# Optimization experiments

Measured on AMD Instinct MI355X. Metric: run time of the kernel, lower is better.

Reference implementation:

```python
import jax, jax.numpy as jnp
import numpy as np


def setup_inputs() -> dict:
    key = jax.random.key(0)
    k1, k2 = jax.random.split(key)
    B, C, Q, D = 32, 4096, 512, 512
    similarity_matrix = jax.random.normal(k1, (B, C, Q), dtype=jnp.float32)
    encoded_question = jax.random.normal(k2, (B, Q, D), dtype=jnp.float32)
    return {"similarity_matrix": similarity_matrix, "encoded_question": encoded_question}


def reference(similarity_matrix, encoded_question):
    # softmax over query axis, then attention-weighted sum of question encodings.
    # Equivalent to the original expand_dims/multiply/sum, but fused as a matmul.
    attn = jax.nn.softmax(similarity_matrix, axis=-1)          # [B, C, Q]
    out = jnp.einsum('bcq,bqd->bcd', attn, encoded_question)   # [B, C, D]
    return out
```

## Files before the change

### kernel.cpp

```cpp
#include <hip/hip_runtime.h>
#include <hip/hip_bf16.h>


constexpr int Bn = 32;
constexpr int Cn = 4096;
constexpr int Qn = 512;
constexpr int Dn = 512;
constexpr int BM = 64;

typedef __attribute__((ext_vector_type(8))) short short8;
typedef __attribute__((ext_vector_type(4))) float floatx4;

__device__ __forceinline__ ushort f2bf(float f) {
  union { float f; unsigned u; } v; v.f = f;
  unsigned r = v.u + 0x7FFFu + ((v.u >> 16) & 1u);
  return (ushort)(r >> 16);
}

__global__ __launch_bounds__(256) void transpose_conv(const float* __restrict__ E,
                                                      ushort* __restrict__ Et) {
  __shared__ float tile[32][33];
  int b = blockIdx.z, q0 = blockIdx.y * 32, d0 = blockIdx.x * 32;
  int x = threadIdx.x & 31, y = threadIdx.x >> 5;
  const float* src = E + ((size_t)b * Qn + q0) * Dn + d0;
#pragma unroll
  for (int k = 0; k < 4; ++k)
    tile[y + 8 * k][x] = src[(size_t)(y + 8 * k) * Dn + x];
  __syncthreads();
  ushort* dst = Et + ((size_t)b * Dn + d0) * Qn + q0;
#pragma unroll
  for (int k = 0; k < 4; ++k)
    dst[(size_t)(y + 8 * k) * Qn + x] = f2bf(tile[x][y + 8 * k]);
}

__global__ __launch_bounds__(512, 4) void c2q_fused(const float* __restrict__ sim,
                                                    const ushort* __restrict__ Et,
                                                    float* __restrict__ out) {
  __shared__ char Plds[BM * Qn * 2];
  __shared__ float rsInv[BM];

  const int tid  = threadIdx.x;
  const int lane = tid & 63;
  const int wid  = tid >> 6;
  const int l16  = lane & 15;
  const int lhi  = lane >> 4;
  const int b    = blockIdx.y;
  const int c0   = blockIdx.x * BM;

  const int srow = tid >> 3;
  const int skp  = tid & 7;
  const float* sload = sim + ((size_t)b * Cn + c0 + srow) * Qn + skp * 8;

  float4 v[16];
#pragma unroll
  for (int c = 0; c < 8; ++c) {
    v[2 * c]     = *(const float4*)(sload + c * 64);
    v[2 * c + 1] = *(const float4*)(sload + c * 64 + 4);
  }
  float rsum = 0.0f;
#pragma unroll
  for (int c = 0; c < 8; ++c) {
    float e0 = __expf(v[2 * c].x),     e1 = __expf(v[2 * c].y);
    float e2 = __expf(v[2 * c].z),     e3 = __expf(v[2 * c].w);
    float e4 = __expf(v[2 * c + 1].x), e5 = __expf(v[2 * c + 1].y);
    float e6 = __expf(v[2 * c + 1].z), e7 = __expf(v[2 * c + 1].w);
    rsum += ((e0 + e1) + (e2 + e3)) + ((e4 + e5) + (e6 + e7));
    uint4 pk;
    pk.x = (uint)f2bf(e0) | ((uint)f2bf(e1) << 16);
    pk.y = (uint)f2bf(e2) | ((uint)f2bf(e3) << 16);
    pk.z = (uint)f2bf(e4) | ((uint)f2bf(e5) << 16);
    pk.w = (uint)f2bf(e6) | ((uint)f2bf(e7) << 16);
    int off = (srow << 10) + (c << 7) + (skp << 4);
    off ^= (srow & 7) << 4;
    *(uint4*)(Plds + off) = pk;
  }
  rsum += __shfl_xor(rsum, 1);
  rsum += __shfl_xor(rsum, 2);
  rsum += __shfl_xor(rsum, 4);
  if (skp == 0) rsInv[srow] = 1.0f / rsum;
  __syncthreads();

  floatx4 acc[4][4] = {};
  const ushort* EtB = Et + ((size_t)b * Dn + wid * 64 + l16) * Qn + lhi * 8;

  short8 bb[4], nb[4];
#pragma unroll
  for (int nr = 0; nr < 4; ++nr)
    bb[nr] = *(const short8*)(EtB + (size_t)nr * 16 * Qn);

#pragma unroll
  for (int ks = 0; ks < 16; ++ks) {
    if (ks < 15) {
#pragma unroll
      for (int nr = 0; nr < 4; ++nr)
        nb[nr] = *(const short8*)(EtB + (size_t)nr * 16 * Qn + (ks + 1) * 32);
    }
    short8 a[4];
#pragma unroll
    for (int mr = 0; mr < 4; ++mr) {
      int row = mr * 16 + l16;
      int off = (row << 10) + (ks << 6) + (lhi << 4);
      off ^= (row & 7) << 4;
      a[mr] = *(const short8*)(Plds + off);
    }
    __builtin_amdgcn_s_setprio(1);
#pragma unroll
    for (int mr = 0; mr < 4; ++mr)
#pragma unroll
      for (int nr = 0; nr < 4; ++nr)
        acc[mr][nr] = __builtin_amdgcn_mfma_f32_16x16x32_bf16(a[mr], bb[nr],
                                                              acc[mr][nr], 0, 0, 0);
    __builtin_amdgcn_s_setprio(0);
#pragma unroll
    for (int nr = 0; nr < 4; ++nr) bb[nr] = nb[nr];
  }

  float* outp = out + ((size_t)b * Cn + c0) * Dn;
#pragma unroll
  for (int mr = 0; mr < 4; ++mr) {
    float rs[4];
#pragma unroll
    for (int rr = 0; rr < 4; ++rr) rs[rr] = rsInv[mr * 16 + lhi * 4 + rr];
#pragma unroll
    for (int nr = 0; nr < 4; ++nr) {
      int col = wid * 64 + nr * 16 + l16;
#pragma unroll
      for (int rr = 0; rr < 4; ++rr) {
        int row = mr * 16 + lhi * 4 + rr;
        outp[(size_t)row * Dn + col] = acc[mr][nr][rr] * rs[rr];
      }
    }
  }
}

extern "C" void kernel_launch(void* const* d_in, const int* in_sizes, int n_in,
                              void* d_out, int out_size, void* d_ws, size_t ws_size,
                              hipStream_t stream) {
  const float* sim = (const float*)d_in[0];
  const float* enc = (const float*)d_in[1];
  float* outp = (float*)d_out;
  ushort* Et = (ushort*)d_ws;

  transpose_conv<<<dim3(Dn / 32, Qn / 32, Bn), 256, 0, stream>>>(enc, Et);
  c2q_fused<<<dim3(Cn / BM, Bn), 512, 0, stream>>>(sim, Et, outp);
}
```

Baseline: 205.1 us.

## Make c2q blocks persistent over row subtiles with double-buffered softmax staging

```diff
diff --git a/kernel.cpp b/kernel.cpp
--- a/kernel.cpp
+++ b/kernel.cpp
@@ -6,7 +6,9 @@
 constexpr int Cn = 4096;
 constexpr int Qn = 512;
 constexpr int Dn = 512;
-constexpr int BM = 64;
+constexpr int BM = 32;
+constexpr int NSUB = 8;
+constexpr int ROWS = BM * NSUB;
 
 typedef __attribute__((ext_vector_type(8))) short short8;
 typedef __attribute__((ext_vector_type(4))) float floatx4;
@@ -36,100 +38,123 @@
 __global__ __launch_bounds__(512, 4) void c2q_fused(const float* __restrict__ sim,
                                                     const ushort* __restrict__ Et,
                                                     float* __restrict__ out) {
-  __shared__ char Plds[BM * Qn * 2];
-  __shared__ float rsInv[BM];
+  __shared__ char Pbuf[2][BM * Qn * 2];
+  __shared__ float rsInv[2][BM];
 
   const int tid  = threadIdx.x;
   const int lane = tid & 63;
   const int wid  = tid >> 6;
   const int l16  = lane & 15;
   const int lhi  = lane >> 4;
-  const int b    = blockIdx.y;
-  const int c0   = blockIdx.x * BM;
 
-  const int srow = tid >> 3;
-  const int skp  = tid & 7;
-  const float* sload = sim + ((size_t)b * Cn + c0 + srow) * Qn + skp * 8;
+  const int b  = blockIdx.x & 31;
+  const int c0 = (blockIdx.x >> 5) * ROWS;
 
-  float4 v[16];
+  const int srow = tid >> 4;
+  const int skp  = tid & 15;
+  const float* sload = sim + ((size_t)b * Cn + c0 + srow) * Qn + skp * 4;
+  const int swz = (srow & 7) << 4;
+
+  float4 v[8];
+
 #pragma unroll
-  for (int c = 0; c < 8; ++c) {
-    v[2 * c]     = *(const float4*)(sload + c * 64);
-    v[2 * c + 1] = *(const float4*)(sload + c * 64 + 4);
+  for (int j = 0; j < 8; ++j) v[j] = *(const float4*)(sload + j * 64);
+  {
+    float rsum = 0.0f;
+#pragma unroll
+    for (int j = 0; j < 8; ++j) {
+      float e0 = __expf(v[j].x), e1 = __expf(v[j].y);
+      float e2 = __expf(v[j].z), e3 = __expf(v[j].w);
+      rsum += (e0 + e1) + (e2 + e3);
+      uint2 pk;
+      pk.x = (uint)f2bf(e0) | ((uint)f2bf(e1) << 16);
+      pk.y = (uint)f2bf(e2) | ((uint)f2bf(e3) << 16);
+      *(uint2*)(Pbuf[0] + (((srow << 10) + (j << 7) + (skp << 3)) ^ swz)) = pk;
+    }
+    rsum += __shfl_xor(rsum, 1);
+    rsum += __shfl_xor(rsum, 2);
+    rsum += __shfl_xor(rsum, 4);
+    rsum += __shfl_xor(rsum, 8);
+    if (skp == 0) rsInv[0][srow] = 1.0f / rsum;
   }
-  float rsum = 0.0f;
-#pragma unroll
-  for (int c = 0; c < 8; ++c) {
-    float e0 = __expf(v[2 * c].x),     e1 = __expf(v[2 * c].y);
-    float e2 = __expf(v[2 * c].z),     e3 = __expf(v[2 * c].w);
-    float e4 = __expf(v[2 * c + 1].x), e5 = __expf(v[2 * c + 1].y);
-    float e6 = __expf(v[2 * c + 1].z), e7 = __expf(v[2 * c + 1].w);
-    rsum += ((e0 + e1) + (e2 + e3)) + ((e4 + e5) + (e6 + e7));
-    uint4 pk;
-    pk.x = (uint)f2bf(e0) | ((uint)f2bf(e1) << 16);
-    pk.y = (uint)f2bf(e2) | ((uint)f2bf(e3) << 16);
-    pk.z = (uint)f2bf(e4) | ((uint)f2bf(e5) << 16);
-    pk.w = (uint)f2bf(e6) | ((uint)f2bf(e7) << 16);
-    int off = (srow << 10) + (c << 7) + (skp << 4);
-    off ^= (srow & 7) << 4;
-    *(uint4*)(Plds + off) = pk;
-  }
-  rsum += __shfl_xor(rsum, 1);
-  rsum += __shfl_xor(rsum, 2);
-  rsum += __shfl_xor(rsum, 4);
-  if (skp == 0) rsInv[srow] = 1.0f / rsum;
   __syncthreads();
 
-  floatx4 acc[4][4] = {};
   const ushort* EtB = Et + ((size_t)b * Dn + wid * 64 + l16) * Qn + lhi * 8;
-
-  short8 bb[4], nb[4];
+  short8 bb[4];
 #pragma unroll
   for (int nr = 0; nr < 4; ++nr)
     bb[nr] = *(const short8*)(EtB + (size_t)nr * 16 * Qn);
 
+  for (int t = 0; t < NSUB; ++t) {
+    if (t < NSUB - 1) {
+      const float* nl = sload + (size_t)(t + 1) * BM * Qn;
 #pragma unroll
-  for (int ks = 0; ks < 16; ++ks) {
-    if (ks < 15) {
+      for (int j = 0; j < 8; ++j) v[j] = *(const float4*)(nl + j * 64);
+    }
+    __builtin_amdgcn_sched_barrier(0);
+
+    floatx4 acc[2][4] = {};
+    const char* pb = Pbuf[t & 1];
+#pragma unroll
+    for (int ks = 0; ks < 16; ++ks) {
+      short8 nb[4];
 #pragma unroll
       for (int nr = 0; nr < 4; ++nr)
-        nb[nr] = *(const short8*)(EtB + (size_t)nr * 16 * Qn + (ks + 1) * 32);
+        nb[nr] = *(const short8*)(EtB + (size_t)nr * 16 * Qn + ((ks + 1) & 15) * 32);
+      short8 a[2];
+#pragma unroll
+      for (int mr = 0; mr < 2; ++mr) {
+        int row = mr * 16 + l16;
+        int off = ((row << 10) + (ks << 6) + (lhi << 4)) ^ ((row & 7) << 4);
+        a[mr] = *(const short8*)(pb + off);
+      }
+      __builtin_amdgcn_s_setprio(1);
+#pragma unroll
+      for (int mr = 0; mr < 2; ++mr)
+#pragma unroll
+        for (int nr = 0; nr < 4; ++nr)
+          acc[mr][nr] = __builtin_amdgcn_mfma_f32_16x16x32_bf16(a[mr], bb[nr],
+                                                                acc[mr][nr], 0, 0, 0);
+      __builtin_amdgcn_s_setprio(0);
+#pragma unroll
+      for (int nr = 0; nr < 4; ++nr) bb[nr] = nb[nr];
     }
-    short8 a[4];
+
+    float* outp = out + ((size_t)b * Cn + c0 + t * BM) * Dn;
 #pragma unroll
-    for (int mr = 0; mr < 4; ++mr) {
-      int row = mr * 16 + l16;
-      int off = (row << 10) + (ks << 6) + (lhi << 4);
-      off ^= (row & 7) << 4;
-      a[mr] = *(const short8*)(Plds + off);
-    }
-    __builtin_amdgcn_s_setprio(1);
+    for (int mr = 0; mr < 2; ++mr) {
+      float rs[4];
 #pragma unroll
-    for (int mr = 0; mr < 4; ++mr)
+      for (int rr = 0; rr < 4; ++rr) rs[rr] = rsInv[t & 1][mr * 16 + lhi * 4 + rr];
 #pragma unroll
-      for (int nr = 0; nr < 4; ++nr)
-        acc[mr][nr] = __builtin_amdgcn_mfma_f32_16x16x32_bf16(a[mr], bb[nr],
-                                                              acc[mr][nr], 0, 0, 0);
-    __builtin_amdgcn_s_setprio(0);
+      for (int nr = 0; nr < 4; ++nr) {
+        int col = wid * 64 + nr * 16 + l16;
 #pragma unroll
-    for (int nr = 0; nr < 4; ++nr) bb[nr] = nb[nr];
-  }
-
-  float* outp = out + ((size_t)b * Cn + c0) * Dn;
-#pragma unroll
-  for (int mr = 0; mr < 4; ++mr) {
-    float rs[4];
-#pragma unroll
-    for (int rr = 0; rr < 4; ++rr) rs[rr] = rsInv[mr * 16 + lhi * 4 + rr];
-#pragma unroll
-    for (int nr = 0; nr < 4; ++nr) {
-      int col = wid * 64 + nr * 16 + l16;
-#pragma unroll
-      for (int rr = 0; rr < 4; ++rr) {
-        int row = mr * 16 + lhi * 4 + rr;
-        outp[(size_t)row * Dn + col] = acc[mr][nr][rr] * rs[rr];
+        for (int rr = 0; rr < 4; ++rr)
+          outp[(size_t)(mr * 16 + lhi * 4 + rr) * Dn + col] = acc[mr][nr][rr] * rs[rr];
       }
     }
+
+    if (t < NSUB - 1) {
+      float rsum = 0.0f;
+      char* wb = Pbuf[(t + 1) & 1];
+#pragma unroll
+      for (int j = 0; j < 8; ++j) {
+        float e0 = __expf(v[j].x), e1 = __expf(v[j].y);
+        float e2 = __expf(v[j].z), e3 = __expf(v[j].w);
+        rsum += (e0 + e1) + (e2 + e3);
+        uint2 pk;
+        pk.x = (uint)f2bf(e0) | ((uint)f2bf(e1) << 16);
+        pk.y = (uint)f2bf(e2) | ((uint)f2bf(e3) << 16);
+        *(uint2*)(wb + (((srow << 10) + (j << 7) + (skp << 3)) ^ swz)) = pk;
+      }
+      rsum += __shfl_xor(rsum, 1);
+      rsum += __shfl_xor(rsum, 2);
+      rsum += __shfl_xor(rsum, 4);
+      rsum += __shfl_xor(rsum, 8);
+      if (skp == 0) rsInv[(t + 1) & 1][srow] = 1.0f / rsum;
+    }
+    __syncthreads();
   }
 }
 
@@ -142,5 +167,5 @@
   ushort* Et = (ushort*)d_ws;
 
   transpose_conv<<<dim3(Dn / 32, Qn / 32, Bn), 256, 0, stream>>>(enc, Et);
-  c2q_fused<<<dim3(Cn / BM, Bn), 512, 0, stream>>>(sim, Et, outp);
+  c2q_fused<<<dim3((Cn / ROWS) * Bn), 512, 0, stream>>>(sim, Et, outp);
 }
```

Result: slower. 742.2 us (+261.8%).

## Pipeline softmax exp with MFMA, prepack encoder into fragment layout

Applied to the files above, without the earlier changes.

```diff
diff --git a/kernel.cpp b/kernel.cpp
--- a/kernel.cpp
+++ b/kernel.cpp
@@ -6,7 +6,6 @@
 constexpr int Cn = 4096;
 constexpr int Qn = 512;
 constexpr int Dn = 512;
-constexpr int BM = 64;
 
 typedef __attribute__((ext_vector_type(8))) short short8;
 typedef __attribute__((ext_vector_type(4))) float floatx4;
@@ -17,105 +16,129 @@
   return (ushort)(r >> 16);
 }
 
-__global__ __launch_bounds__(256) void transpose_conv(const float* __restrict__ E,
-                                                      ushort* __restrict__ Et) {
-  __shared__ float tile[32][33];
-  int b = blockIdx.z, q0 = blockIdx.y * 32, d0 = blockIdx.x * 32;
-  int x = threadIdx.x & 31, y = threadIdx.x >> 5;
-  const float* src = E + ((size_t)b * Qn + q0) * Dn + d0;
-#pragma unroll
-  for (int k = 0; k < 4; ++k)
-    tile[y + 8 * k][x] = src[(size_t)(y + 8 * k) * Dn + x];
-  __syncthreads();
-  ushort* dst = Et + ((size_t)b * Dn + d0) * Qn + q0;
-#pragma unroll
-  for (int k = 0; k < 4; ++k)
-    dst[(size_t)(y + 8 * k) * Qn + x] = f2bf(tile[x][y + 8 * k]);
+__device__ __forceinline__ uint4 exp_pack(float4 x, float4 y, float& rsum) {
+  float e0 = __expf(x.x), e1 = __expf(x.y), e2 = __expf(x.z), e3 = __expf(x.w);
+  float e4 = __expf(y.x), e5 = __expf(y.y), e6 = __expf(y.z), e7 = __expf(y.w);
+  rsum += ((e0 + e1) + (e2 + e3)) + ((e4 + e5) + (e6 + e7));
+  uint4 pk;
+  pk.x = (uint)f2bf(e0) | ((uint)f2bf(e1) << 16);
+  pk.y = (uint)f2bf(e2) | ((uint)f2bf(e3) << 16);
+  pk.z = (uint)f2bf(e4) | ((uint)f2bf(e5) << 16);
+  pk.w = (uint)f2bf(e6) | ((uint)f2bf(e7) << 16);
+  return pk;
 }
 
-__global__ __launch_bounds__(512, 4) void c2q_fused(const float* __restrict__ sim,
-                                                    const ushort* __restrict__ Et,
+__global__ __launch_bounds__(256) void enc_to_frag(const float* __restrict__ E,
+                                                   ushort* __restrict__ Etf) {
+  const int ks = blockIdx.x, b = blockIdx.y;
+  const int t = threadIdx.x;
+  const int lane = t & 63, grp = t >> 6;
+  const int l16 = lane & 15, lhi = lane >> 4;
+  const float* src = E + ((size_t)b * Qn + ks * 32 + lhi * 8) * Dn + l16;
+#pragma unroll
+  for (int dt8 = 0; dt8 < 8; ++dt8) {
+    int dt = grp * 8 + dt8;
+    float e[8];
+#pragma unroll
+    for (int j = 0; j < 8; ++j) e[j] = src[(size_t)j * Dn + dt * 16];
+    uint4 pk;
+    pk.x = (uint)f2bf(e[0]) | ((uint)f2bf(e[1]) << 16);
+    pk.y = (uint)f2bf(e[2]) | ((uint)f2bf(e[3]) << 16);
+    pk.z = (uint)f2bf(e[4]) | ((uint)f2bf(e[5]) << 16);
+    pk.w = (uint)f2bf(e[6]) | ((uint)f2bf(e[7]) << 16);
+    *(uint4*)((char*)Etf + (((size_t)(b * 32 + dt) * 16 + ks) * 64 + lane) * 16) = pk;
+  }
+}
+
+__global__ __launch_bounds__(512, 2) void c2q_fused(const float* __restrict__ sim,
+                                                    const ushort* __restrict__ Etf,
                                                     float* __restrict__ out) {
-  __shared__ char Plds[BM * Qn * 2];
-  __shared__ float rsInv[BM];
+  __shared__ char Abuf[2][64 * 128];
+  __shared__ float rsInv[64];
 
   const int tid  = threadIdx.x;
   const int lane = tid & 63;
   const int wid  = tid >> 6;
   const int l16  = lane & 15;
   const int lhi  = lane >> 4;
-  const int b    = blockIdx.y;
-  const int c0   = blockIdx.x * BM;
+
+  const int lin = blockIdx.x;
+  const int blo = lin & 7;
+  const int bhi = (lin >> 3) & 3;
+  const int mt  = lin >> 5;
+  const int b   = bhi * 8 + blo;
+  const int c0  = mt * 64;
 
   const int srow = tid >> 3;
-  const int skp  = tid & 7;
-  const float* sload = sim + ((size_t)b * Cn + c0 + srow) * Qn + skp * 8;
+  const int so   = tid & 7;
+  const float* sload = sim + ((size_t)b * Cn + c0 + srow) * Qn + so * 8;
+  const int swa = (srow * 128 + so * 16) ^ ((srow & 7) << 4);
 
-  float4 v[16];
+  const short8* EB = (const short8*)Etf + ((size_t)(b * 32 + wid * 4) * 16) * 64 + lane;
+
+  float rsum = 0.0f;
+  floatx4 acc[4][4] = {};
+  float4 vs[2][2];
+  short8 bfr[2][4];
+
+  vs[0][0] = *(const float4*)(sload);
+  vs[0][1] = *(const float4*)(sload + 4);
+  vs[1][0] = *(const float4*)(sload + 64);
+  vs[1][1] = *(const float4*)(sload + 68);
 #pragma unroll
-  for (int c = 0; c < 8; ++c) {
-    v[2 * c]     = *(const float4*)(sload + c * 64);
-    v[2 * c + 1] = *(const float4*)(sload + c * 64 + 4);
+  for (int nr = 0; nr < 4; ++nr) {
+    bfr[0][nr] = EB[((size_t)nr * 16 + 0) * 64];
+    bfr[1][nr] = EB[((size_t)nr * 16 + 1) * 64];
   }
-  float rsum = 0.0f;
-#pragma unroll
-  for (int c = 0; c < 8; ++c) {
-    float e0 = __expf(v[2 * c].x),     e1 = __expf(v[2 * c].y);
-    float e2 = __expf(v[2 * c].z),     e3 = __expf(v[2 * c].w);
-    float e4 = __expf(v[2 * c + 1].x), e5 = __expf(v[2 * c + 1].y);
-    float e6 = __expf(v[2 * c + 1].z), e7 = __expf(v[2 * c + 1].w);
-    rsum += ((e0 + e1) + (e2 + e3)) + ((e4 + e5) + (e6 + e7));
-    uint4 pk;
-    pk.x = (uint)f2bf(e0) | ((uint)f2bf(e1) << 16);
-    pk.y = (uint)f2bf(e2) | ((uint)f2bf(e3) << 16);
-    pk.z = (uint)f2bf(e4) | ((uint)f2bf(e5) << 16);
-    pk.w = (uint)f2bf(e6) | ((uint)f2bf(e7) << 16);
-    int off = (srow << 10) + (c << 7) + (skp << 4);
-    off ^= (srow & 7) << 4;
-    *(uint4*)(Plds + off) = pk;
-  }
-  rsum += __shfl_xor(rsum, 1);
-  rsum += __shfl_xor(rsum, 2);
-  rsum += __shfl_xor(rsum, 4);
-  if (skp == 0) rsInv[srow] = 1.0f / rsum;
+  *(uint4*)(Abuf[0] + swa) = exp_pack(vs[0][0], vs[0][1], rsum);
   __syncthreads();
 
-  floatx4 acc[4][4] = {};
-  const ushort* EtB = Et + ((size_t)b * Dn + wid * 64 + l16) * Qn + lhi * 8;
-
-  short8 bb[4], nb[4];
 #pragma unroll
-  for (int nr = 0; nr < 4; ++nr)
-    bb[nr] = *(const short8*)(EtB + (size_t)nr * 16 * Qn);
+  for (int t = 0; t < 8; ++t) {
+    if (t < 6) {
+      vs[t & 1][0] = *(const float4*)(sload + (t + 2) * 64);
+      vs[t & 1][1] = *(const float4*)(sload + (t + 2) * 64 + 4);
+    }
+    __builtin_amdgcn_sched_barrier(0);
 
 #pragma unroll
-  for (int ks = 0; ks < 16; ++ks) {
-    if (ks < 15) {
+    for (int ks = 0; ks < 2; ++ks) {
+      const int kidx = 2 * t + ks;
+      short8 a[4];
 #pragma unroll
-      for (int nr = 0; nr < 4; ++nr)
-        nb[nr] = *(const short8*)(EtB + (size_t)nr * 16 * Qn + (ks + 1) * 32);
+      for (int mr = 0; mr < 4; ++mr) {
+        int row = mr * 16 + l16;
+        a[mr] = *(const short8*)(Abuf[t & 1] +
+                 ((row * 128 + ks * 64 + lhi * 16) ^ ((row & 7) << 4)));
+      }
+      __builtin_amdgcn_s_setprio(1);
+#pragma unroll
+      for (int mr = 0; mr < 4; ++mr)
+#pragma unroll
+        for (int nr = 0; nr < 4; ++nr)
+          acc[mr][nr] = __builtin_amdgcn_mfma_f32_16x16x32_bf16(
+              a[mr], bfr[kidx & 1][nr], acc[mr][nr], 0, 0, 0);
+      __builtin_amdgcn_s_setprio(0);
+      if (kidx < 14) {
+#pragma unroll
+        for (int nr = 0; nr < 4; ++nr)
+          bfr[kidx & 1][nr] = EB[((size_t)nr * 16 + kidx + 2) * 64];
+      }
     }
-    short8 a[4];
-#pragma unroll
-    for (int mr = 0; mr < 4; ++mr) {
-      int row = mr * 16 + l16;
-      int off = (row << 10) + (ks << 6) + (lhi << 4);
-      off ^= (row & 7) << 4;
-      a[mr] = *(const short8*)(Plds + off);
+
+    if (t < 7) {
+      *(uint4*)(Abuf[(t + 1) & 1] + swa) =
+          exp_pack(vs[(t + 1) & 1][0], vs[(t + 1) & 1][1], rsum);
+    } else {
+      rsum += __shfl_xor(rsum, 1);
+      rsum += __shfl_xor(rsum, 2);
+      rsum += __shfl_xor(rsum, 4);
+      if (so == 0) rsInv[srow] = 1.0f / rsum;
     }
-    __builtin_amdgcn_s_setprio(1);
-#pragma unroll
-    for (int mr = 0; mr < 4; ++mr)
-#pragma unroll
-      for (int nr = 0; nr < 4; ++nr)
-        acc[mr][nr] = __builtin_amdgcn_mfma_f32_16x16x32_bf16(a[mr], bb[nr],
-                                                              acc[mr][nr], 0, 0, 0);
-    __builtin_amdgcn_s_setprio(0);
-#pragma unroll
-    for (int nr = 0; nr < 4; ++nr) bb[nr] = nb[nr];
+    __syncthreads();
   }
 
-  float* outp = out + ((size_t)b * Cn + c0) * Dn;
+  float* outp = out + ((size_t)b * Cn + c0) * Dn + wid * 64;
 #pragma unroll
   for (int mr = 0; mr < 4; ++mr) {
     float rs[4];
@@ -123,11 +146,10 @@
     for (int rr = 0; rr < 4; ++rr) rs[rr] = rsInv[mr * 16 + lhi * 4 + rr];
 #pragma unroll
     for (int nr = 0; nr < 4; ++nr) {
-      int col = wid * 64 + nr * 16 + l16;
 #pragma unroll
       for (int rr = 0; rr < 4; ++rr) {
         int row = mr * 16 + lhi * 4 + rr;
-        outp[(size_t)row * Dn + col] = acc[mr][nr][rr] * rs[rr];
+        outp[(size_t)row * Dn + nr * 16 + l16] = acc[mr][nr][rr] * rs[rr];
       }
     }
   }
@@ -139,8 +161,8 @@
   const float* sim = (const float*)d_in[0];
   const float* enc = (const float*)d_in[1];
   float* outp = (float*)d_out;
-  ushort* Et = (ushort*)d_ws;
+  ushort* Etf = (ushort*)d_ws;
 
-  transpose_conv<<<dim3(Dn / 32, Qn / 32, Bn), 256, 0, stream>>>(enc, Et);
-  c2q_fused<<<dim3(Cn / BM, Bn), 512, 0, stream>>>(sim, Et, outp);
+  enc_to_frag<<<dim3(16, Bn), 256, 0, stream>>>(enc, Etf);
+  c2q_fused<<<dim3(2048), 512, 0, stream>>>(sim, Etf, outp);
 }
```

Result: faster. 165.6 us (-19.3%).
